# Performance work log

Measured on AMD Instinct MI355X. Metric: run time of the kernel, lower is better.

## Reference

```python
import jax, jax.numpy as jnp
import numpy as np

ALPHA = 5.0   # ATan surrogate sharpness
THETA = 1.0   # firing threshold
EPS = 1e-5    # BatchNorm eps

@jax.custom_vjp
def spike(x):
    # forward: heaviside; backward: ATan surrogate
    return (x >= 0.0).astype(x.dtype)

def _spike_fwd(x):
    return spike(x), x

def _spike_bwd(x, g):
    return (g * (ALPHA / 2.0) / (1.0 + (jnp.pi / 2.0 * ALPHA * x) ** 2),)

spike.defvjp(_spike_fwd, _spike_bwd)

def lif_layer(x, W, beta_p, gamma, bias, U0):
    # x: [B,T,J], W: [I,J] -> h: [B,T,I]
    h = jnp.einsum('btj,ij->bti', x, W)
    # BatchNorm1d in training mode: per-channel stats over B*T (biased var)
    mu = h.mean(axis=(0, 1))
    var = h.var(axis=(0, 1))
    h = (h - mu) * jax.lax.rsqrt(var + EPS) * gamma + bias
    beta = jax.nn.sigmoid(beta_p)  # [I]
    S0 = jnp.zeros_like(U0)

    def step(carry, xt):
        Ut, St = carry
        Ut = beta * (Ut - THETA * St) + (1.0 - beta) * xt  # soft reset
        St = spike(Ut - THETA)
        return (Ut, St), St

    _, o = jax.lax.scan(step, (U0, S0), jnp.swapaxes(h, 0, 1))  # [T,B,I]
    return jnp.swapaxes(o, 0, 1)  # [B,T,I]

def setup_inputs() -> dict:
    key = jax.random.key(0)
    B, T, J, H = 32, 1024, 1024, 2048
    ks = jax.random.split(key, 16)
    f32 = jnp.float32
    inp = {
        'x': jax.random.normal(ks[0], (B, T, J), f32),
        'W1': jax.random.normal(ks[1], (H, J), f32) / np.sqrt(J),
        'beta1': jax.random.uniform(ks[2], (H,), f32, 0.0, 4.0),
        'gamma1': jnp.ones((H,), f32),
        'bias1': jnp.zeros((H,), f32),
        'U01': jax.random.uniform(ks[3], (B, H), f32),
        'W2': jax.random.normal(ks[4], (H, H), f32) / np.sqrt(H),
        'beta2': jax.random.uniform(ks[5], (H,), f32, 0.0, 4.0),
        'gamma2': jnp.ones((H,), f32),
        'bias2': jnp.zeros((H,), f32),
        'U02': jax.random.uniform(ks[6], (B, H), f32),
        'W3': jax.random.normal(ks[7], (J, H), f32) / np.sqrt(H),
        'beta3': jax.random.uniform(ks[8], (J,), f32, 0.0, 4.0),
        'gamma3': jnp.ones((J,), f32),
        'bias3': jnp.zeros((J,), f32),
        'U03': jax.random.uniform(ks[9], (B, J), f32),
    }
    return inp

def reference(x, W1, beta1, gamma1, bias1, U01,
              W2, beta2, gamma2, bias2, U02,
              W3, beta3, gamma3, bias3, U03):
    h = lif_layer(x, W1, beta1, gamma1, bias1, U01)
    h = lif_layer(h, W2, beta2, gamma2, bias2, U02)
    h = lif_layer(h, W3, beta3, gamma3, bias3, U03)
    return h
```

## Files before the change

### kernel.cpp

```cpp
#include <hip/hip_runtime.h>
#include <hip/hip_bf16.h>
#include <cmath>

#define BB 32
#define TT 1024
#define JJ 1024
#define HH 2048
#define MM (BB * TT)
#define MHALF (MM / 2)

typedef short s8v __attribute__((ext_vector_type(8)));
typedef float f4v __attribute__((ext_vector_type(4)));
typedef unsigned int u4v __attribute__((ext_vector_type(4)));
union ABu { u4v u; s8v v; };

__device__ inline void split_bf16x3(float w, unsigned short& h,
                                    unsigned short& m, unsigned short& l) {
    __hip_bfloat16 bh = __float2bfloat16(w);
    const float fh = __bfloat162float(bh);
    const float r1 = w - fh;
    __hip_bfloat16 bm = __float2bfloat16(r1);
    const float fm = __bfloat162float(bm);
    __hip_bfloat16 bl = __float2bfloat16(r1 - fm);
    h = *(unsigned short*)&bh; m = *(unsigned short*)&bm; l = *(unsigned short*)&bl;
}

__global__ void split_w(const float* __restrict__ W,
                        unsigned short* __restrict__ ph,
                        unsigned short* __restrict__ pm,
                        unsigned short* __restrict__ pl, int n)
{
    const int i = blockIdx.x * 256 + threadIdx.x;
    if (i >= n) return;
    split_bf16x3(W[i], ph[i], pm[i], pl[i]);
}

__global__ __launch_bounds__(512) void mfma_spk_gemm(
    const unsigned long long* __restrict__ S,
    int Mstr,
    const unsigned short* __restrict__ Wh,
    const unsigned short* __restrict__ Wm,
    const unsigned short* __restrict__ Wl,
    float* __restrict__ C, int M, int N, int K)
{
    __shared__ __align__(16) unsigned short Blds[2][3][2][64][32];
    __shared__ __align__(16) unsigned long long Alds[2][512];
    const int tid = threadIdx.x;
    const int wv = tid >> 6;
    const int lane = tid & 63;
    const int wm = wv >> 1, wn = wv & 1;
    const int r16 = lane & 15, quad = lane >> 4;
    const int bm = blockIdx.x * 512;
    const int bn = blockIdx.y * 64;

    f4v acc[8][2] = {};

    const int rl = lane >> 2, chl = lane & 3;
    const unsigned short* sW[3];
    size_t sOff[3];
    int sP[3], sKh[3], sQ[3];
#pragma unroll
    for (int i = 0; i < 3; ++i) {
        const int e = wv * 3 + i;
        const int p = e >> 3, kh = (e >> 2) & 1, q = e & 3;
        const int srow = q * 16 + rl;
        const int kc = (chl - (srow >> 1)) & 3;
        sW[i] = (p == 0) ? Wh : (p == 1) ? Wm : Wl;
        sOff[i] = (size_t)(bn + srow) * K + kh * 32 + kc * 8;
        sP[i] = p; sKh[i] = kh; sQ[i] = q;
    }

    int arow[8];
#pragma unroll
    for (int ms = 0; ms < 8; ++ms) arow[ms] = wm * 128 + ms * 16 + r16;

    int bR[2], bC[2];
#pragma unroll
    for (int ns = 0; ns < 2; ++ns) {
        bR[ns] = wn * 32 + ns * 16 + r16;
        bC[ns] = ((quad + (bR[ns] >> 1)) & 3) * 8;
    }

    auto stageB = [&](int buf, int i, int k0) {
        __builtin_amdgcn_global_load_lds(
            (const __attribute__((address_space(1))) void*)(sW[i] + sOff[i] + k0),
            (__attribute__((address_space(3))) void*)&Blds[buf][sP[i]][sKh[i]][sQ[i] * 16][0],
            16, 0, 0);
    };
    auto stageA = [&](int buf, int tk) {
        if (wv < 4)
            __builtin_amdgcn_global_load_lds(
                (const __attribute__((address_space(1))) void*)
                    (S + (size_t)tk * Mstr + bm + wv * 128 + lane * 2),
                (__attribute__((address_space(3))) void*)&Alds[buf][wv * 128],
                16, 0, 0);
    };

    stageA(0, 0);
#pragma unroll
    for (int i = 0; i < 3; ++i) stageB(0, i, 0);
    __syncthreads();

    const int NT = K >> 6;
    for (int t = 0; t < NT; ++t) {
        const int cur = t & 1, nxt = cur ^ 1;

        if (t + 1 < NT) {
            stageA(nxt, t + 1);
#pragma unroll
            for (int i = 0; i < 3; ++i) stageB(nxt, i, (t + 1) << 6);
        }

        s8v afr[2][8];
#pragma unroll
        for (int ms = 0; ms < 8; ++ms) {
            const unsigned long long a64 = Alds[cur][arow[ms]];
            const unsigned int w0 = (unsigned int)a64;
            const unsigned int w1 = (unsigned int)(a64 >> 32);
#pragma unroll
            for (int kh = 0; kh < 2; ++kh) {
                const unsigned int b = ((kh ? w1 : w0) >> (quad * 8)) & 0xFFu;
                ABu tu;
                tu.u[0] = ((b        & 1u) * 0x3F80u) | (((b >> 1) & 1u) * 0x3F800000u);
                tu.u[1] = (((b >> 2) & 1u) * 0x3F80u) | (((b >> 3) & 1u) * 0x3F800000u);
                tu.u[2] = (((b >> 4) & 1u) * 0x3F80u) | (((b >> 5) & 1u) * 0x3F800000u);
                tu.u[3] = (((b >> 6) & 1u) * 0x3F80u) | (((b >> 7) & 1u) * 0x3F800000u);
                afr[kh][ms] = tu.v;
            }
        }

#pragma unroll
        for (int p = 0; p < 3; ++p)
#pragma unroll
            for (int kh = 0; kh < 2; ++kh) {
                s8v bf[2];
#pragma unroll
                for (int ns = 0; ns < 2; ++ns)
                    bf[ns] = *(const s8v*)&Blds[cur][p][kh][bR[ns]][bC[ns]];
                __builtin_amdgcn_s_setprio(1);
#pragma unroll
                for (int ms = 0; ms < 8; ++ms)
#pragma unroll
                    for (int ns = 0; ns < 2; ++ns)
                        acc[ms][ns] = __builtin_amdgcn_mfma_f32_16x16x32_bf16(
                            afr[kh][ms], bf[ns], acc[ms][ns], 0, 0, 0);
                __builtin_amdgcn_s_setprio(0);
            }

        if (t + 1 < NT) __syncthreads();
    }

#pragma unroll
    for (int ms = 0; ms < 8; ++ms)
#pragma unroll
        for (int ns = 0; ns < 2; ++ns) {
            const int row = bm + wm * 128 + ms * 16 + quad * 4;
            const int col = bn + wn * 32 + ns * 16 + r16;
#pragma unroll
            for (int r = 0; r < 4; ++r)
                C[(size_t)(row + r) * N + col] = acc[ms][ns][r];
        }
}

struct Sp3 { unsigned int o0, o1, o2; };

__device__ inline Sp3 split_pair(float x, float y)
{
    const unsigned int xb = __float_as_uint(x), yb = __float_as_uint(y);
    const unsigned int x0 = xb & 0xFFFF0000u,  y0 = yb & 0xFFFF0000u;
    const float xr1 = x - __uint_as_float(x0), yr1 = y - __uint_as_float(y0);
    const unsigned int x1b = __float_as_uint(xr1), y1b = __float_as_uint(yr1);
    const unsigned int x1 = x1b & 0xFFFF0000u, y1 = y1b & 0xFFFF0000u;
    const float xr2 = xr1 - __uint_as_float(x1), yr2 = yr1 - __uint_as_float(y1);
    Sp3 r;
    r.o0 = __builtin_amdgcn_perm(yb, xb, 0x07060302u);
    r.o1 = __builtin_amdgcn_perm(y1b, x1b, 0x07060302u);
    r.o2 = __builtin_amdgcn_perm(__float_as_uint(yr2), __float_as_uint(xr2), 0x07060302u);
    return r;
}

__global__ __launch_bounds__(256) void mfma_f32x3_gemm(
    const float* __restrict__ A,
    const unsigned short* __restrict__ Wh,
    const unsigned short* __restrict__ Wm,
    const unsigned short* __restrict__ Wl,
    float* __restrict__ C, int M, int N, int K)
{
    __shared__ __align__(16) unsigned short Blds[2][3][128][32];
    const int tid = threadIdx.x;
    const int wv = tid >> 6;
    const int lane = tid & 63;
    const int wm = wv >> 1, wn = wv & 1;
    const int r16 = lane & 15, quad = lane >> 4;

    const int lin = blockIdx.y * 16 + blockIdx.x;
    const int ppx = gridDim.y >> 3;
    const int xcd = lin & 7, li = lin >> 3;
    const int pm = xcd * ppx + (li >> 4);
    const int pn = li & 15;
    const int bm = pm * 128;
    const int bn = pn * 128;

    f4v acc[4][4] = {};

    const int rl = lane >> 2, chl = lane & 3;
    size_t soff[2];
    int ldsrow[2];
#pragma unroll
    for (int i = 0; i < 2; ++i) {
        const int r = i * 64 + wv * 16 + rl;
        const int kc = (chl - (r >> 1)) & 3;
        soff[i] = (size_t)(bn + r) * K + kc * 8;
        ldsrow[i] = i * 64 + wv * 16;
    }

    size_t aoff[4];
#pragma unroll
    for (int ms = 0; ms < 4; ++ms)
        aoff[ms] = (size_t)(bm + wm * 64 + ms * 16 + r16) * K + quad * 8;

    int bR[4], bC[4];
#pragma unroll
    for (int ns = 0; ns < 4; ++ns) {
        bR[ns] = wn * 64 + ns * 16 + r16;
        bC[ns] = ((quad + (bR[ns] >> 1)) & 3) * 8;
    }

    auto stage = [&](int buf, int p, int i, int k0) {
        const unsigned short* Wp = (p == 0) ? Wh : (p == 1) ? Wm : Wl;
        __builtin_amdgcn_global_load_lds(
            (const __attribute__((address_space(1))) void*)(Wp + soff[i] + k0),
            (__attribute__((address_space(3))) void*)&Blds[buf][p][ldsrow[i]][0], 16, 0, 0);
    };

    float4 av[4][2];
#pragma unroll
    for (int ms = 0; ms < 4; ++ms) {
        av[ms][0] = *(const float4*)(A + aoff[ms]);
        av[ms][1] = *(const float4*)(A + aoff[ms] + 4);
    }
#pragma unroll
    for (int p = 0; p < 3; ++p)
#pragma unroll
        for (int i = 0; i < 2; ++i) stage(0, p, i, 0);
    __syncthreads();

    const int NT = K >> 5;
    for (int t = 0; t < NT; ++t) {
        const int cur = t & 1, nxt = cur ^ 1;
        const int k0 = t << 5;

        if (t + 1 < NT) {
#pragma unroll
            for (int p = 0; p < 3; ++p)
#pragma unroll
                for (int i = 0; i < 2; ++i) stage(nxt, p, i, k0 + 32);
        }

        s8v afr[3][4];
#pragma unroll
        for (int ms = 0; ms < 4; ++ms) {
            ABu t0, t1, t2;
            const float4 v0 = av[ms][0];
            const float4 v1 = av[ms][1];
            const Sp3 s0 = split_pair(v0.x, v0.y);
            const Sp3 s1 = split_pair(v0.z, v0.w);
            const Sp3 s2 = split_pair(v1.x, v1.y);
            const Sp3 s3 = split_pair(v1.z, v1.w);
            t0.u[0] = s0.o0; t1.u[0] = s0.o1; t2.u[0] = s0.o2;
            t0.u[1] = s1.o0; t1.u[1] = s1.o1; t2.u[1] = s1.o2;
            t0.u[2] = s2.o0; t1.u[2] = s2.o1; t2.u[2] = s2.o2;
            t0.u[3] = s3.o0; t1.u[3] = s3.o1; t2.u[3] = s3.o2;
            afr[0][ms] = t0.v;
            afr[1][ms] = t1.v;
            afr[2][ms] = t2.v;
        }
        if (t + 1 < NT) {
#pragma unroll
            for (int ms = 0; ms < 4; ++ms) {
                av[ms][0] = *(const float4*)(A + aoff[ms] + k0 + 32);
                av[ms][1] = *(const float4*)(A + aoff[ms] + k0 + 32 + 4);
            }
        }

#pragma unroll
        for (int pw = 0; pw < 3; ++pw) {
            s8v bf[4];
#pragma unroll
            for (int ns = 0; ns < 4; ++ns)
                bf[ns] = *(const s8v*)&Blds[cur][pw][bR[ns]][bC[ns]];
            __builtin_amdgcn_s_setprio(1);
#pragma unroll
            for (int pa = 0; pa + pw < 3; ++pa)
#pragma unroll
                for (int ms = 0; ms < 4; ++ms)
#pragma unroll
                    for (int ns = 0; ns < 4; ++ns)
                        acc[ms][ns] = __builtin_amdgcn_mfma_f32_16x16x32_bf16(
                            afr[pa][ms], bf[ns], acc[ms][ns], 0, 0, 0);
            __builtin_amdgcn_s_setprio(0);
        }

        if (t + 1 < NT) __syncthreads();
    }

#pragma unroll
    for (int ms = 0; ms < 4; ++ms)
#pragma unroll
        for (int ns = 0; ns < 4; ++ns) {
            const int row = bm + wm * 64 + ms * 16 + quad * 4;
            const int col = bn + wn * 64 + ns * 16 + r16;
#pragma unroll
            for (int r = 0; r < 4; ++r)
                C[(size_t)(row + r) * N + col] = acc[ms][ns][r];
        }
}

#define RCHUNK 128

__global__ void bn_stats_partial2(const float* __restrict__ hA,
                                  const float* __restrict__ hB,
                                  float* __restrict__ partial, int N)
{
    const int n = blockIdx.x * 256 + threadIdx.x;
    const int chunk = blockIdx.y;
    const int half = (MM / RCHUNK) / 2;
    const float* __restrict__ h = (chunk < half) ? hA : hB;
    const int cl = chunk & (half - 1);
    const float* p = h + (size_t)cl * RCHUNK * N + n;
    float s = 0.f, s2 = 0.f;
#pragma unroll 4
    for (int r = 0; r < RCHUNK; ++r) {
        const float v = p[(size_t)r * N];
        s += v;
        s2 = fmaf(v, v, s2);
    }
    partial[((size_t)chunk * 2 + 0) * N + n] = s;
    partial[((size_t)chunk * 2 + 1) * N + n] = s2;
}

__global__ void bn_stats_final(const float* __restrict__ partial,
                               float* __restrict__ stats,
                               int N, int nchunks)
{
    const int n = blockIdx.x * 256 + threadIdx.x;
    double s = 0.0, s2 = 0.0;
    for (int c = 0; c < nchunks; ++c) {
        s  += (double)partial[((size_t)c * 2 + 0) * N + n];
        s2 += (double)partial[((size_t)c * 2 + 1) * N + n];
    }
    const double inv_m = 1.0 / (double)MM;
    const double mu = s * inv_m;
    const double var = s2 * inv_m - mu * mu;
    stats[n]     = (float)mu;
    stats[N + n] = (float)(1.0 / sqrt(var + 1e-5));
}

#define LIF_STEP_PACK(hv)                                            \
    do {                                                             \
        const float hn = ((hv) - mu) * rstd * g + bi;                \
        u = beta * (u - s) + omb * hn;                               \
        const bool sp = (u - 1.0f) >= 0.f;                           \
        s = sp ? 1.f : 0.f;                                          \
        const unsigned long long mball = __ballot(sp);               \
        if (lead) bits[widx] = mball;                                \
        ++widx;                                                      \
    } while (0)

#define LIF_LOAD8(buf, tbase)                                        \
    _Pragma("unroll")                                                \
    for (int j = 0; j < 8; ++j) {                                    \
        const int tl = (tbase) + j;                                  \
        buf[j] = h[base + (size_t)(tl < TT ? tl : TT - 1) * N];      \
    }

__global__ __launch_bounds__(64) void bn_lif_scan_pack2(
    const float* __restrict__ hA,
    const float* __restrict__ hB,
    unsigned long long* __restrict__ bits,
    const float* __restrict__ stats,
    const float* __restrict__ gamma,
    const float* __restrict__ bias,
    const float* __restrict__ beta_p,
    const float* __restrict__ U0,
    int N)
{
    const int n = blockIdx.x * 64 + threadIdx.x;
    const int b = blockIdx.y;
    const float* __restrict__ h = (b < BB / 2) ? hA : hB;
    const int bl = b & (BB / 2 - 1);
    const float mu = stats[n];
    const float rstd = stats[N + n];
    const float g = gamma[n];
    const float bi = bias[n];
    const float beta = 1.f / (1.f + expf(-beta_p[n]));
    const float omb = 1.f - beta;
    float u = U0[(size_t)b * N + n];
    float s = 0.f;
    const size_t base = ((size_t)bl * TT) * N + n;
    size_t widx = (size_t)(n >> 6) * (size_t)MM + (size_t)b * TT;
    const bool lead = (threadIdx.x & 63) == 0;

    float b0[8], b1[8], b2[8], b3[8];
    LIF_LOAD8(b0, 0);
    LIF_LOAD8(b1, 8);
    LIF_LOAD8(b2, 16);
    for (int t0 = 0; t0 < TT; t0 += 32) {
        LIF_LOAD8(b3, t0 + 24);
#pragma unroll
        for (int j = 0; j < 8; ++j) { const float hv = b0[j]; LIF_STEP_PACK(hv); }
        LIF_LOAD8(b0, t0 + 32);
#pragma unroll
        for (int j = 0; j < 8; ++j) { const float hv = b1[j]; LIF_STEP_PACK(hv); }
        LIF_LOAD8(b1, t0 + 40);
#pragma unroll
        for (int j = 0; j < 8; ++j) { const float hv = b2[j]; LIF_STEP_PACK(hv); }
        LIF_LOAD8(b2, t0 + 48);
#pragma unroll
        for (int j = 0; j < 8; ++j) { const float hv = b3[j]; LIF_STEP_PACK(hv); }
    }
}

#define LIF_STEP_F32(hv)                                             \
    do {                                                             \
        const float hn = ((hv) - mu) * rstd * g + bi;                \
        u = beta * (u - s) + omb * hn;                               \
        s = ((u - 1.0f) >= 0.f) ? 1.f : 0.f;                         \
        out[oidx] = s;                                               \
        oidx += N;                                                   \
    } while (0)

__global__ __launch_bounds__(64) void bn_lif_scan_f32_2(
    const float* __restrict__ h,
    float* __restrict__ out,
    const float* __restrict__ stats,
    const float* __restrict__ gamma,
    const float* __restrict__ bias,
    const float* __restrict__ beta_p,
    const float* __restrict__ U0,
    int N)
{
    const int n = blockIdx.x * 64 + threadIdx.x;
    const int b = blockIdx.y;
    const float mu = stats[n];
    const float rstd = stats[N + n];
    const float g = gamma[n];
    const float bi = bias[n];
    const float beta = 1.f / (1.f + expf(-beta_p[n]));
    const float omb = 1.f - beta;
    float u = U0[(size_t)b * N + n];
    float s = 0.f;
    const size_t base = ((size_t)b * TT) * N + n;
    size_t oidx = base;

    float b0[8], b1[8], b2[8], b3[8];
    LIF_LOAD8(b0, 0);
    LIF_LOAD8(b1, 8);
    LIF_LOAD8(b2, 16);
    for (int t0 = 0; t0 < TT; t0 += 32) {
        LIF_LOAD8(b3, t0 + 24);
#pragma unroll
        for (int j = 0; j < 8; ++j) { const float hv = b0[j]; LIF_STEP_F32(hv); }
        LIF_LOAD8(b0, t0 + 32);
#pragma unroll
        for (int j = 0; j < 8; ++j) { const float hv = b1[j]; LIF_STEP_F32(hv); }
        LIF_LOAD8(b1, t0 + 40);
#pragma unroll
        for (int j = 0; j < 8; ++j) { const float hv = b2[j]; LIF_STEP_F32(hv); }
        LIF_LOAD8(b2, t0 + 48);
#pragma unroll
        for (int j = 0; j < 8; ++j) { const float hv = b3[j]; LIF_STEP_F32(hv); }
    }
}

extern "C" void kernel_launch(void* const* d_in, const int* in_sizes, int n_in,
                              void* d_out, int out_size, void* d_ws, size_t ws_size,
                              hipStream_t stream)
{
    const float* x   = (const float*)d_in[0];
    const float* W1  = (const float*)d_in[1];
    const float* bp1 = (const float*)d_in[2];
    const float* g1  = (const float*)d_in[3];
    const float* bi1 = (const float*)d_in[4];
    const float* U01 = (const float*)d_in[5];
    const float* W2  = (const float*)d_in[6];
    const float* bp2 = (const float*)d_in[7];
    const float* g2  = (const float*)d_in[8];
    const float* bi2 = (const float*)d_in[9];
    const float* U02 = (const float*)d_in[10];
    const float* W3  = (const float*)d_in[11];
    const float* bp3 = (const float*)d_in[12];
    const float* g3  = (const float*)d_in[13];
    const float* bi3 = (const float*)d_in[14];
    const float* U03 = (const float*)d_in[15];
    float* out = (float*)d_out;

    unsigned char* ws = (unsigned char*)d_ws;
    const size_t HA_BYTES  = (size_t)MHALF * HH * sizeof(float);
    const size_t SPK_BYTES = (size_t)MM * (HH / 8);
    float*              hA   = (float*)ws;
    float*              hB   = (float*)d_out;
    unsigned long long* spk  = (unsigned long long*)(ws + HA_BYTES);
    float*              part = (float*)(ws + HA_BYTES + SPK_BYTES);
    float*              stat = (float*)(ws + HA_BYTES + SPK_BYTES + 4194304);
    unsigned short*     W2h  = (unsigned short*)(ws + HA_BYTES + SPK_BYTES + 4194304 + 16384);
    unsigned short*     W2m  = W2h + (size_t)HH * HH;
    unsigned short*     W2l  = W2m + (size_t)HH * HH;
    unsigned short*     W3h  = W2l + (size_t)HH * HH;
    unsigned short*     W3m  = W3h + (size_t)JJ * HH;
    unsigned short*     W3l  = W3m + (size_t)JJ * HH;

    const dim3 blk(256);
    const dim3 blk64(64);
    const dim3 blk512(512);
    const int nck = MM / RCHUNK;

    split_w<<<dim3((HH * JJ) / 256), blk, 0, stream>>>(W1, W2h, W2m, W2l, HH * JJ);
    mfma_f32x3_gemm<<<dim3(HH / 128, MHALF / 128), blk, 0, stream>>>(
        x, W2h, W2m, W2l, hA, MHALF, HH, JJ);
    mfma_f32x3_gemm<<<dim3(HH / 128, MHALF / 128), blk, 0, stream>>>(
        x + (size_t)MHALF * JJ, W2h, W2m, W2l, hB, MHALF, HH, JJ);
    split_w<<<dim3((HH * HH) / 256), blk, 0, stream>>>(W2, W2h, W2m, W2l, HH * HH);
    split_w<<<dim3((JJ * HH) / 256), blk, 0, stream>>>(W3, W3h, W3m, W3l, JJ * HH);

    bn_stats_partial2<<<dim3(HH / 256, nck), blk, 0, stream>>>(hA, hB, part, HH);
    bn_stats_final<<<dim3(HH / 256), blk, 0, stream>>>(part, stat, HH, nck);
    bn_lif_scan_pack2<<<dim3(HH / 64, BB), blk64, 0, stream>>>(
        hA, hB, spk, stat, g1, bi1, bp1, U01, HH);

    mfma_spk_gemm<<<dim3(MHALF / 512, HH / 64), blk512, 0, stream>>>(
        spk, MM, W2h, W2m, W2l, hA, MHALF, HH, HH);
    mfma_spk_gemm<<<dim3(MHALF / 512, HH / 64), blk512, 0, stream>>>(
        spk + MHALF, MM, W2h, W2m, W2l, hB, MHALF, HH, HH);
    bn_stats_partial2<<<dim3(HH / 256, nck), blk, 0, stream>>>(hA, hB, part, HH);
    bn_stats_final<<<dim3(HH / 256), blk, 0, stream>>>(part, stat, HH, nck);
    bn_lif_scan_pack2<<<dim3(HH / 64, BB), blk64, 0, stream>>>(
        hA, hB, spk, stat, g2, bi2, bp2, U02, HH);

    mfma_spk_gemm<<<dim3(MM / 512, JJ / 64), blk512, 0, stream>>>(
        spk, MM, W3h, W3m, W3l, hA, MM, JJ, HH);
    bn_stats_partial2<<<dim3(JJ / 256, nck), blk, 0, stream>>>(
        hA, hA + (size_t)MHALF * JJ, part, JJ);
    bn_stats_final<<<dim3(JJ / 256), blk, 0, stream>>>(part, stat, JJ, nck);
    bn_lif_scan_f32_2<<<dim3(JJ / 64, BB), blk64, 0, stream>>>(
        hA, out, stat, g3, bi3, bp3, U03, JJ);
}
```

Measured before the change: 2.463 ms.

## Overlap next-tile prefetch with compute using partial vmcnt waits in spike GEMM

Replaces the full __syncthreads waits with an explicit s_waitcnt vmcnt(5), so each iteration waits only for the current tile's global-to-LDS loads while the next tile's loads stay in flight. The A staging is also redistributed: every wave issues two 4-byte global_load_lds calls instead of four waves issuing one 16-byte call each, which gives all waves the same number of loads for the counter arithmetic. The risks are correctness if the vmcnt count does not match the loads actually issued, and the smaller 4-byte transfers for A.

After: 2.485 ms. Within noise of the previous version (+0.9%).

```diff
diff --git a/kernel.cpp b/kernel.cpp
--- a/kernel.cpp
+++ b/kernel.cpp
@@ -87,29 +87,40 @@
             (__attribute__((address_space(3))) void*)&Blds[buf][sP[i]][sKh[i]][sQ[i] * 16][0],
             16, 0, 0);
     };
-    auto stageA = [&](int buf, int tk) {
-        if (wv < 4)
-            __builtin_amdgcn_global_load_lds(
-                (const __attribute__((address_space(1))) void*)
-                    (S + (size_t)tk * Mstr + bm + wv * 128 + lane * 2),
-                (__attribute__((address_space(3))) void*)&Alds[buf][wv * 128],
-                16, 0, 0);
+    auto stageA = [&](int buf, int i, int tk) {
+        const unsigned int* src =
+            (const unsigned int*)(S + (size_t)tk * Mstr + bm)
+            + (wv * 2 + i) * 64 + lane;
+        __builtin_amdgcn_global_load_lds(
+            (const __attribute__((address_space(1))) void*)src,
+            (__attribute__((address_space(3))) void*)
+                ((unsigned int*)&Alds[buf][0] + (wv * 2 + i) * 64),
+            4, 0, 0);
     };
 
-    stageA(0, 0);
 #pragma unroll
     for (int i = 0; i < 3; ++i) stageB(0, i, 0);
-    __syncthreads();
+#pragma unroll
+    for (int i = 0; i < 2; ++i) stageA(0, i, 0);
 
     const int NT = K >> 6;
     for (int t = 0; t < NT; ++t) {
         const int cur = t & 1, nxt = cur ^ 1;
 
         if (t + 1 < NT) {
-            stageA(nxt, t + 1);
 #pragma unroll
             for (int i = 0; i < 3; ++i) stageB(nxt, i, (t + 1) << 6);
-        }
+#pragma unroll
+            for (int i = 0; i < 2; ++i) stageA(nxt, i, t + 1);
+            __builtin_amdgcn_sched_barrier(0);
+            asm volatile("s_waitcnt vmcnt(5)" ::: "memory");
+        } else {
+            __builtin_amdgcn_sched_barrier(0);
+            asm volatile("s_waitcnt vmcnt(0)" ::: "memory");
+        }
+        __builtin_amdgcn_sched_barrier(0);
+        __builtin_amdgcn_s_barrier();
+        __builtin_amdgcn_sched_barrier(0);
 
         s8v afr[2][8];
 #pragma unroll
@@ -147,7 +158,8 @@
                 __builtin_amdgcn_s_setprio(0);
             }
 
-        if (t + 1 < NT) __syncthreads();
+        __builtin_amdgcn_sched_barrier(0);
+        __builtin_amdgcn_s_barrier();
     }
 
 #pragma unroll
```

## Load spike bitmask A operand directly into registers and speed bit expansion

Applied to the files above, without the earlier changes.

Removes the LDS staging buffer for the packed spike matrix. Each lane now loads its own 64-bit spike words from global memory into registers, double-buffered by unrolling the K loop by two. The per-byte bit-to-bf16 expansion is rewritten with a multiply-mask bit spread plus v_perm, replacing many shifts and ands. This cuts LDS traffic and ALU work in the inner loop, at the cost of more registers and redundant global loads across lanes that share a row.

Result: faster. 2.314 ms (-6.1%).

```diff
diff --git a/kernel.cpp b/kernel.cpp
--- a/kernel.cpp
+++ b/kernel.cpp
@@ -44,7 +44,6 @@
     float* __restrict__ C, int M, int N, int K)
 {
     __shared__ __align__(16) unsigned short Blds[2][3][2][64][32];
-    __shared__ __align__(16) unsigned long long Alds[2][512];
     const int tid = threadIdx.x;
     const int wv = tid >> 6;
     const int lane = tid & 63;
@@ -52,6 +51,7 @@
     const int r16 = lane & 15, quad = lane >> 4;
     const int bm = blockIdx.x * 512;
     const int bn = blockIdx.y * 64;
+    const unsigned int q8 = quad * 8;
 
     f4v acc[8][2] = {};
 
@@ -70,9 +70,10 @@
         sP[i] = p; sKh[i] = kh; sQ[i] = q;
     }
 
-    int arow[8];
-#pragma unroll
-    for (int ms = 0; ms < 8; ++ms) arow[ms] = wm * 128 + ms * 16 + r16;
+    size_t abase[8];
+#pragma unroll
+    for (int ms = 0; ms < 8; ++ms)
+        abase[ms] = (size_t)(bm + wm * 128 + ms * 16 + r16);
 
     int bR[2], bC[2];
 #pragma unroll
@@ -87,68 +88,70 @@
             (__attribute__((address_space(3))) void*)&Blds[buf][sP[i]][sKh[i]][sQ[i] * 16][0],
             16, 0, 0);
     };
-    auto stageA = [&](int buf, int tk) {
-        if (wv < 4)
-            __builtin_amdgcn_global_load_lds(
-                (const __attribute__((address_space(1))) void*)
-                    (S + (size_t)tk * Mstr + bm + wv * 128 + lane * 2),
-                (__attribute__((address_space(3))) void*)&Alds[buf][wv * 128],
-                16, 0, 0);
-    };
-
-    stageA(0, 0);
+
+    const int NT = K >> 6;
+
+    unsigned long long a64A[8], a64B[8];
+#pragma unroll
+    for (int ms = 0; ms < 8; ++ms) a64A[ms] = S[abase[ms]];
 #pragma unroll
     for (int i = 0; i < 3; ++i) stageB(0, i, 0);
     __syncthreads();
 
-    const int NT = K >> 6;
-    for (int t = 0; t < NT; ++t) {
-        const int cur = t & 1, nxt = cur ^ 1;
-
-        if (t + 1 < NT) {
-            stageA(nxt, t + 1);
-#pragma unroll
-            for (int i = 0; i < 3; ++i) stageB(nxt, i, (t + 1) << 6);
-        }
-
-        s8v afr[2][8];
-#pragma unroll
-        for (int ms = 0; ms < 8; ++ms) {
-            const unsigned long long a64 = Alds[cur][arow[ms]];
-            const unsigned int w0 = (unsigned int)a64;
-            const unsigned int w1 = (unsigned int)(a64 >> 32);
-#pragma unroll
-            for (int kh = 0; kh < 2; ++kh) {
-                const unsigned int b = ((kh ? w1 : w0) >> (quad * 8)) & 0xFFu;
-                ABu tu;
-                tu.u[0] = ((b        & 1u) * 0x3F80u) | (((b >> 1) & 1u) * 0x3F800000u);
-                tu.u[1] = (((b >> 2) & 1u) * 0x3F80u) | (((b >> 3) & 1u) * 0x3F800000u);
-                tu.u[2] = (((b >> 4) & 1u) * 0x3F80u) | (((b >> 5) & 1u) * 0x3F800000u);
-                tu.u[3] = (((b >> 6) & 1u) * 0x3F80u) | (((b >> 7) & 1u) * 0x3F800000u);
-                afr[kh][ms] = tu.v;
-            }
-        }
-
-#pragma unroll
-        for (int p = 0; p < 3; ++p)
-#pragma unroll
-            for (int kh = 0; kh < 2; ++kh) {
-                s8v bf[2];
-#pragma unroll
-                for (int ns = 0; ns < 2; ++ns)
-                    bf[ns] = *(const s8v*)&Blds[cur][p][kh][bR[ns]][bC[ns]];
-                __builtin_amdgcn_s_setprio(1);
-#pragma unroll
-                for (int ms = 0; ms < 8; ++ms)
-#pragma unroll
-                    for (int ns = 0; ns < 2; ++ns)
-                        acc[ms][ns] = __builtin_amdgcn_mfma_f32_16x16x32_bf16(
-                            afr[kh][ms], bf[ns], acc[ms][ns], 0, 0, 0);
-                __builtin_amdgcn_s_setprio(0);
-            }
-
-        if (t + 1 < NT) __syncthreads();
-    }
+#define SPK_STEP(CURA, NXTA, CURL, NXTL, T)                                  \
+    do {                                                                     \
+        if ((T) + 1 < NT) {                                                  \
+            _Pragma("unroll")                                                \
+            for (int i = 0; i < 3; ++i) stageB((NXTL), i, ((T) + 1) << 6);   \
+            _Pragma("unroll")                                                \
+            for (int ms = 0; ms < 8; ++ms)                                   \
+                NXTA[ms] = S[(size_t)((T) + 1) * Mstr + abase[ms]];          \
+        }                                                                    \
+        s8v afr[2][8];                                                       \
+        _Pragma("unroll")                                                    \
+        for (int ms = 0; ms < 8; ++ms) {                                     \
+            const unsigned int w0 = (unsigned int)CURA[ms];                  \
+            const unsigned int w1 = (unsigned int)(CURA[ms] >> 32);          \
+            _Pragma("unroll")                                                \
+            for (int kh = 0; kh < 2; ++kh) {                                 \
+                const unsigned int w = kh ? w1 : w0;                         \
+                const unsigned int bl = (w >> q8) & 0xFu;                    \
+                const unsigned int bh = (w >> (q8 + 4)) & 0xFu;              \
+                const unsigned int lo = (bl * 0x00204081u) & 0x01010101u;    \
+                const unsigned int hi = (bh * 0x00204081u) & 0x01010101u;    \
+                ABu tu;                                                      \
+                tu.u[0] = __builtin_amdgcn_perm(0u, lo, 0x04010400u) * 0x3F80u; \
+                tu.u[1] = __builtin_amdgcn_perm(0u, lo, 0x04030402u) * 0x3F80u; \
+                tu.u[2] = __builtin_amdgcn_perm(0u, hi, 0x04010400u) * 0x3F80u; \
+                tu.u[3] = __builtin_amdgcn_perm(0u, hi, 0x04030402u) * 0x3F80u; \
+                afr[kh][ms] = tu.v;                                          \
+            }                                                                \
+        }                                                                    \
+        _Pragma("unroll")                                                    \
+        for (int p = 0; p < 3; ++p)                                          \
+            _Pragma("unroll")                                                \
+            for (int kh = 0; kh < 2; ++kh) {                                 \
+                s8v bf[2];                                                   \
+                _Pragma("unroll")                                            \
+                for (int ns = 0; ns < 2; ++ns)                               \
+                    bf[ns] = *(const s8v*)&Blds[CURL][p][kh][bR[ns]][bC[ns]];\
+                __builtin_amdgcn_s_setprio(1);                               \
+                _Pragma("unroll")                                            \
+                for (int ms = 0; ms < 8; ++ms)                               \
+                    _Pragma("unroll")                                        \
+                    for (int ns = 0; ns < 2; ++ns)                           \
+                        acc[ms][ns] = __builtin_amdgcn_mfma_f32_16x16x32_bf16( \
+                            afr[kh][ms], bf[ns], acc[ms][ns], 0, 0, 0);      \
+                __builtin_amdgcn_s_setprio(0);                               \
+            }                                                                \
+        if ((T) + 1 < NT) __syncthreads();                                   \
+    } while (0)
+
+    for (int t = 0; t < NT; t += 2) {
+        SPK_STEP(a64A, a64B, 0, 1, t);
+        SPK_STEP(a64B, a64A, 1, 0, t + 1);
+    }
+#undef SPK_STEP
 
 #pragma unroll
     for (int ms = 0; ms < 8; ++ms)
```
